# Optimization experiments

Measured on AMD Instinct MI355X. Metric: run time of the kernel, lower is better.

## Reference

```python
import jax, jax.numpy as jnp
import numpy as np

N = 50000        # nodes
E = 800_000      # edges (avg degree 16)
D_IN, D_HID, D_OUT = 512, 512, 256
P_DROP = 0.5


def setup_inputs() -> dict:
    key = jax.random.key(0)
    k0, k1, k2, k3 = jax.random.split(key, 4)
    x = jax.random.normal(k0, (N, D_IN), dtype=jnp.float32)
    edge_index = jax.random.randint(k1, (2, E), 0, N, dtype=jnp.int64)
    W1 = jax.random.normal(k2, (D_HID, D_IN), dtype=jnp.float32) * 0.02
    b1 = jnp.zeros((D_HID,), dtype=jnp.float32)
    W2 = jax.random.normal(k3, (D_OUT, D_HID), dtype=jnp.float32) * 0.02
    b2 = jnp.zeros((D_OUT,), dtype=jnp.float32)
    return {"x": x, "edge_index": edge_index, "W1": W1, "b1": b1, "W2": W2, "b2": b2}


def _gcn_norm(edge_index, n):
    # add self loops, then symmetric GCN normalization: D^-1/2 (A+I) D^-1/2
    src, dst = edge_index[0], edge_index[1]
    loops = jnp.arange(n, dtype=src.dtype)
    src = jnp.concatenate([src, loops])
    dst = jnp.concatenate([dst, loops])
    deg = jax.ops.segment_sum(jnp.ones_like(src, dtype=jnp.float32), dst, num_segments=n)
    dinv = jax.lax.rsqrt(deg)  # deg >= 1 because of self loops
    norm = dinv[src] * dinv[dst]  # [E+N]
    return src, dst, norm


def _propagate(x, src, dst, norm):
    # out[i] = sum_{(j->i)} norm_e * x[j]
    return jax.ops.segment_sum(x[src] * norm[:, None], dst, num_segments=x.shape[0])


def reference(x, edge_index, W1, b1, W2, b2):
    src, dst, norm = _gcn_norm(edge_index, x.shape[0])
    # SGConv layer 1 (K=1): propagate then linear
    h = _propagate(x, src, dst, norm) @ W1.T + b1
    h = jax.nn.relu(h)
    # F.dropout(p) with training=True default -> deterministic fixed-key mask here
    keep = jax.random.bernoulli(jax.random.key(42), 1.0 - P_DROP, h.shape)
    embedding = jnp.where(keep, h / (1.0 - P_DROP), 0.0)
    # SGConv layer 2
    out = _propagate(embedding, src, dst, norm) @ W2.T + b2
    return embedding, out
```

## Files before the change

### kernel.cpp

```cpp
#include <hip/hip_runtime.h>

typedef unsigned short u16t;
typedef __attribute__((ext_vector_type(8))) short short8;
typedef __attribute__((ext_vector_type(4))) float f32x4;
typedef __attribute__((ext_vector_type(4))) unsigned short u16x4;

__device__ __forceinline__ float bf2f(short b) {
  return __uint_as_float(((unsigned)(unsigned short)b) << 16);
}
__device__ __forceinline__ u16t f2bf(float f) {
  unsigned u = __float_as_uint(f);
  u += 0x7FFFu + ((u >> 16) & 1u);
  return (u16t)(u >> 16);
}

__device__ __forceinline__ bool keep_mask(unsigned flat) {
  const unsigned k0 = 0u, k1 = 42u;
  const unsigned k2 = k0 ^ k1 ^ 0x1BD11BDAu;
  unsigned x0 = 0u + k0;
  unsigned x1 = flat + k1;
#define TF_R(r) { x0 += x1; x1 = (x1 << r) | (x1 >> (32 - r)); x1 ^= x0; }
  TF_R(13) TF_R(15) TF_R(26) TF_R(6)  x0 += k1; x1 += k2 + 1u;
  TF_R(17) TF_R(29) TF_R(16) TF_R(24) x0 += k2; x1 += k0 + 2u;
  TF_R(13) TF_R(15) TF_R(26) TF_R(6)  x0 += k0; x1 += k1 + 3u;
  TF_R(17) TF_R(29) TF_R(16) TF_R(24) x0 += k1; x1 += k2 + 4u;
  TF_R(13) TF_R(15) TF_R(26) TF_R(6)  x0 += k2; x1 += k0 + 5u;
#undef TF_R
  return ((x0 ^ x1) >> 31) == 0u;
}

__device__ __forceinline__ void load_lds16(const u16t* g, u16t* l) {
  __builtin_amdgcn_global_load_lds((__attribute__((address_space(1))) void*)g,
                                   (__attribute__((address_space(3))) void*)l,
                                   16, 0, 0);
}

__global__ void cvt_bf16(const float* __restrict__ s, u16t* __restrict__ d, int n) {
  int i = (blockIdx.x * 256 + threadIdx.x) * 4;
  if (i < n) {
    f32x4 v = *(const f32x4*)&s[i];
    u16x4 o = { f2bf(v.x), f2bf(v.y), f2bf(v.z), f2bf(v.w) };
    *(u16x4*)&d[i] = o;
  }
}

__global__ void count_edges(const int* __restrict__ dst, int E, int* __restrict__ cnt) {
  int e = blockIdx.x * 256 + threadIdx.x;
  if (e < E) atomicAdd(&cnt[dst[e]], 1);
}

__global__ __launch_bounds__(256) void rowp_build(const int* __restrict__ cnt,
    int* __restrict__ rowp, int* __restrict__ cursor, float* __restrict__ dinv,
    int* __restrict__ gctr, int n) {
  __shared__ int sd[256];
  __shared__ int sbase;
  const int tid = threadIdx.x;
  const int i = blockIdx.x * 256 + tid;
  int c = (i < n) ? cnt[i] : 0;
  int v = c;
  sd[tid] = v;
  __syncthreads();
  for (int o = 1; o < 256; o <<= 1) {
    int t = (tid >= o) ? sd[tid - o] : 0;
    __syncthreads();
    v += t;
    sd[tid] = v;
    __syncthreads();
  }
  if (tid == 255) sbase = atomicAdd(gctr, v);
  __syncthreads();
  if (i < n) {
    int start = sbase + v - c;
    rowp[i] = start;
    cursor[i] = start;
    dinv[i] = rsqrtf((float)(c + 1));
  }
}

__global__ void fill_csr(const int* __restrict__ src, const int* __restrict__ dst, int E,
                         int* __restrict__ cursor, int* __restrict__ col) {
  int e = blockIdx.x * 256 + threadIdx.x;
  if (e < E) {
    int d = dst[e];
    int pos = atomicAdd(&cursor[d], 1);
    col[pos] = src[e];
  }
}

__global__ __launch_bounds__(256) void gemm_bt(const u16t* __restrict__ A,
                                               const u16t* __restrict__ B,
                                               u16t* __restrict__ C,
                                               int K, int Ncols) {
  __shared__ __align__(16) u16t lA[128 * 32];
  __shared__ __align__(16) u16t lB[128 * 32];
  const int tid = threadIdx.x;
  const int wave = tid >> 6, lane = tid & 63;
  const int wm = (wave & 1) * 64, wn = (wave >> 1) * 64;
  const int lrow = lane & 15, lq = lane >> 4;
  const u16t* Ab = A + (size_t)blockIdx.y * 128 * K;
  const u16t* Bb = B + (size_t)blockIdx.x * 128 * K;
  const int r0 = tid >> 2, c0 = (tid & 3) * 8;
  const int ldsOff = __builtin_amdgcn_readfirstlane((tid >> 6) * 512);

  f32x4 acc[4][4];
  const f32x4 zero = {0.f, 0.f, 0.f, 0.f};
#pragma unroll
  for (int mi = 0; mi < 4; ++mi)
#pragma unroll
    for (int ni = 0; ni < 4; ++ni) acc[mi][ni] = zero;

  for (int kt = 0; kt < K; kt += 32) {
    __syncthreads();
    load_lds16(Ab + (size_t)r0 * K + kt + c0, &lA[ldsOff]);
    load_lds16(Ab + (size_t)(r0 + 64) * K + kt + c0, &lA[2048 + ldsOff]);
    load_lds16(Bb + (size_t)r0 * K + kt + c0, &lB[ldsOff]);
    load_lds16(Bb + (size_t)(r0 + 64) * K + kt + c0, &lB[2048 + ldsOff]);
    __syncthreads();
    short8 af[4], bfr[4];
#pragma unroll
    for (int mi = 0; mi < 4; ++mi)
      af[mi] = *(const short8*)&lA[(wm + mi * 16 + lrow) * 32 + lq * 8];
#pragma unroll
    for (int ni = 0; ni < 4; ++ni)
      bfr[ni] = *(const short8*)&lB[(wn + ni * 16 + lrow) * 32 + lq * 8];
#pragma unroll
    for (int mi = 0; mi < 4; ++mi)
#pragma unroll
      for (int ni = 0; ni < 4; ++ni)
        acc[mi][ni] = __builtin_amdgcn_mfma_f32_16x16x32_bf16(af[mi], bfr[ni], acc[mi][ni], 0, 0, 0);
  }

  const size_t crow = (size_t)blockIdx.y * 128 + wm + lq * 4;
  const int ccol = blockIdx.x * 128 + wn + lrow;
#pragma unroll
  for (int mi = 0; mi < 4; ++mi)
#pragma unroll
    for (int r = 0; r < 4; ++r)
#pragma unroll
      for (int ni = 0; ni < 4; ++ni)
        C[(crow + mi * 16 + r) * Ncols + ccol + ni * 16] = f2bf(acc[mi][ni][r]);
}

__global__ __launch_bounds__(256) void prop1_kernel(const u16t* __restrict__ y1,
    const int* __restrict__ col, const int* __restrict__ rowp, const int* __restrict__ rowend,
    const float* __restrict__ dinv, const float* __restrict__ b1,
    float* __restrict__ embf, u16t* __restrict__ embb, int n) {
  const int lane = threadIdx.x & 63;
  const int i = blockIdx.x * 4 + (threadIdx.x >> 6);
  if (i >= n) return;
  const int f = lane * 8;
  const float di = dinv[i];
  float acc[8];
  short8 v = *(const short8*)&y1[(size_t)i * 512 + f];
#pragma unroll
  for (int j = 0; j < 8; ++j) acc[j] = di * bf2f(v[j]);
  int e = rowp[i];
  const int e1 = rowend[i];
  for (; e + 8 <= e1; e += 8) {
    int s[8];
    float w[8];
    short8 u[8];
#pragma unroll
    for (int q = 0; q < 8; ++q) s[q] = col[e + q];
#pragma unroll
    for (int q = 0; q < 8; ++q) w[q] = dinv[s[q]];
#pragma unroll
    for (int q = 0; q < 8; ++q) u[q] = *(const short8*)&y1[(size_t)s[q] * 512 + f];
#pragma unroll
    for (int q = 0; q < 8; ++q)
#pragma unroll
      for (int j = 0; j < 8; ++j) acc[j] += w[q] * bf2f(u[q][j]);
  }
  for (; e + 4 <= e1; e += 4) {
    int s[4];
    float w[4];
    short8 u[4];
#pragma unroll
    for (int q = 0; q < 4; ++q) s[q] = col[e + q];
#pragma unroll
    for (int q = 0; q < 4; ++q) w[q] = dinv[s[q]];
#pragma unroll
    for (int q = 0; q < 4; ++q) u[q] = *(const short8*)&y1[(size_t)s[q] * 512 + f];
#pragma unroll
    for (int q = 0; q < 4; ++q)
#pragma unroll
      for (int j = 0; j < 8; ++j) acc[j] += w[q] * bf2f(u[q][j]);
  }
  for (; e < e1; ++e) {
    const int s = col[e];
    const float w = dinv[s];
    short8 u = *(const short8*)&y1[(size_t)s * 512 + f];
#pragma unroll
    for (int j = 0; j < 8; ++j) acc[j] += w * bf2f(u[j]);
  }
  const unsigned flat = (unsigned)i * 512u + (unsigned)f;
  f32x4 o0, o1;
  short8 ob;
#pragma unroll
  for (int j = 0; j < 8; ++j) {
    float h = di * acc[j] + b1[f + j];
    h = fmaxf(h, 0.f);
    float eb = keep_mask(flat + (unsigned)j) ? 2.f * h : 0.f;
    if (j < 4) o0[j] = eb; else o1[j - 4] = eb;
    ob[j] = (short)f2bf(eb);
  }
  *(f32x4*)&embf[(size_t)i * 512 + f] = o0;
  *(f32x4*)&embf[(size_t)i * 512 + f + 4] = o1;
  *(short8*)&embb[(size_t)i * 512 + f] = ob;
}

__global__ __launch_bounds__(256) void prop2_kernel(const u16t* __restrict__ z,
    const int* __restrict__ col, const int* __restrict__ rowp, const int* __restrict__ rowend,
    const float* __restrict__ dinv, const float* __restrict__ b2,
    float* __restrict__ outp, int n) {
  const int h = threadIdx.x & 31;
  const int i = blockIdx.x * 8 + (threadIdx.x >> 5);
  if (i >= n) return;
  const int f = h * 8;
  const float di = dinv[i];
  float acc[8];
  short8 v = *(const short8*)&z[(size_t)i * 256 + f];
#pragma unroll
  for (int j = 0; j < 8; ++j) acc[j] = di * bf2f(v[j]);
  int e = rowp[i];
  const int e1 = rowend[i];
  for (; e + 4 <= e1; e += 4) {
    int s[4];
    float w[4];
    short8 u[4];
#pragma unroll
    for (int q = 0; q < 4; ++q) s[q] = col[e + q];
#pragma unroll
    for (int q = 0; q < 4; ++q) w[q] = dinv[s[q]];
#pragma unroll
    for (int q = 0; q < 4; ++q) u[q] = *(const short8*)&z[(size_t)s[q] * 256 + f];
#pragma unroll
    for (int q = 0; q < 4; ++q)
#pragma unroll
      for (int j = 0; j < 8; ++j) acc[j] += w[q] * bf2f(u[q][j]);
  }
  for (; e < e1; ++e) {
    const int s = col[e];
    const float w = dinv[s];
    short8 u = *(const short8*)&z[(size_t)s * 256 + f];
#pragma unroll
    for (int j = 0; j < 8; ++j) acc[j] += w * bf2f(u[j]);
  }
  f32x4 o0, o1;
#pragma unroll
  for (int j = 0; j < 8; ++j) {
    float r = di * acc[j] + b2[f + j];
    if (j < 4) o0[j] = r; else o1[j - 4] = r;
  }
  *(f32x4*)&outp[(size_t)i * 256 + f] = o0;
  *(f32x4*)&outp[(size_t)i * 256 + f + 4] = o1;
}

extern "C" void kernel_launch(void* const* d_in, const int* in_sizes, int n_in,
                              void* d_out, int out_size, void* d_ws, size_t ws_size,
                              hipStream_t stream) {
  (void)n_in; (void)out_size; (void)ws_size;
  const float* x  = (const float*)d_in[0];
  const int*   ei = (const int*)d_in[1];
  const float* W1 = (const float*)d_in[2];
  const float* b1 = (const float*)d_in[3];
  const float* W2 = (const float*)d_in[4];
  const float* b2 = (const float*)d_in[5];

  const int Nn = in_sizes[0] / 512;
  const int E  = in_sizes[1] / 2;
  const int Mpad = ((Nn + 127) / 128) * 128;
  const int K = 512;

  char* ws = (char*)d_ws;
  size_t off = 0;
  auto take = [&](size_t bytes) -> char* {
    char* p = ws + off;
    off += (bytes + 255) & ~(size_t)255;
    return p;
  };
  u16t* xb   = (u16t*)take((size_t)Mpad * 512 * 2);
  u16t* y1b  = (u16t*)take((size_t)Mpad * 512 * 2);
  u16t* W1b  = (u16t*)take((size_t)512 * 512 * 2);
  u16t* W2b  = (u16t*)take((size_t)256 * 512 * 2);
  int*   cnt    = (int*)take((size_t)(Nn + 1) * 4);
  int*   rowp   = (int*)take((size_t)Nn * 4);
  int*   cursor = (int*)take((size_t)Nn * 4);
  float* dinv   = (float*)take((size_t)Nn * 4);
  int*   colA   = (int*)take((size_t)E * 4);

  float* embf = (float*)d_out;
  float* outf = (float*)d_out + (size_t)Nn * 512;

  hipMemsetAsync(cnt, 0, (size_t)(Nn + 1) * 4, stream);

  const int n1 = Nn * 512;
  cvt_bf16<<<(n1 / 4 + 255) / 256, 256, 0, stream>>>(x, xb, n1);
  cvt_bf16<<<(512 * 512 / 4 + 255) / 256, 256, 0, stream>>>(W1, W1b, 512 * 512);
  cvt_bf16<<<(256 * 512 / 4 + 255) / 256, 256, 0, stream>>>(W2, W2b, 256 * 512);

  count_edges<<<(E + 255) / 256, 256, 0, stream>>>(ei + E, E, cnt);
  rowp_build<<<(Nn + 255) / 256, 256, 0, stream>>>(cnt, rowp, cursor, dinv, cnt + Nn, Nn);
  fill_csr<<<(E + 255) / 256, 256, 0, stream>>>(ei, ei + E, E, cursor, colA);

  dim3 g1(512 / 128, Mpad / 128);
  gemm_bt<<<g1, 256, 0, stream>>>(xb, W1b, y1b, K, 512);
  prop1_kernel<<<(Nn + 3) / 4, 256, 0, stream>>>(y1b, colA, rowp, cursor, dinv, b1,
                                                 embf, xb , Nn);

  u16t* zb = y1b;
  dim3 g2(256 / 128, Mpad / 128);
  gemm_bt<<<g2, 256, 0, stream>>>(xb, W2b, zb, K, 256);
  prop2_kernel<<<(Nn + 7) / 8, 256, 0, stream>>>(zb, colA, rowp, cursor, dinv, b2, outf, Nn);
}
```

Measured before the change: 591.4 us.

## Split propagation feature dimension across two blocks per node chunk

Both propagation kernels now split each node's feature row into two halves handled by separate blocks. The block index is remapped so that the two halves of a 4-node chunk are launched close together and can share L2 hits on the gathered neighbor rows. Each thread now loads narrower vectors (4 or 2 bf16 values), which doubles the block count and the parallelism available for hiding gather latency. The cost is that the edge indices and dinv values are read twice, and the narrower loads are less efficient per request. prop2 also moves from 32-thread to 64-thread groups per node and gains an 8-way unrolled edge loop.

New measurement: 590.9 us. About the same (-0.1%).

```diff
diff --git a/kernel.cpp b/kernel.cpp
--- a/kernel.cpp
+++ b/kernel.cpp
@@ -2,7 +2,10 @@
 
 typedef unsigned short u16t;
 typedef __attribute__((ext_vector_type(8))) short short8;
+typedef __attribute__((ext_vector_type(4))) short short4v;
+typedef __attribute__((ext_vector_type(2))) short short2v;
 typedef __attribute__((ext_vector_type(4))) float f32x4;
+typedef __attribute__((ext_vector_type(2))) float f32x2;
 typedef __attribute__((ext_vector_type(4))) unsigned short u16x4;
 
 __device__ __forceinline__ float bf2f(short b) {
@@ -144,116 +147,116 @@
 __global__ __launch_bounds__(256) void prop1_kernel(const u16t* __restrict__ y1,
     const int* __restrict__ col, const int* __restrict__ rowp, const int* __restrict__ rowend,
     const float* __restrict__ dinv, const float* __restrict__ b1,
-    float* __restrict__ embf, u16t* __restrict__ embb, int n) {
+    float* __restrict__ embf, u16t* __restrict__ embb, int n, int nchunk) {
+  const int b = blockIdx.x;
+  const int slot = b & 7;
+  const int hf = slot >> 2;
+  const int chunk = (b >> 3) * 4 + (slot & 3);
+  if (chunk >= nchunk) return;
+  const int i = __builtin_amdgcn_readfirstlane(chunk * 4 + (threadIdx.x >> 6));
+  if (i >= n) return;
   const int lane = threadIdx.x & 63;
-  const int i = blockIdx.x * 4 + (threadIdx.x >> 6);
-  if (i >= n) return;
-  const int f = lane * 8;
+  const int f = hf * 256 + lane * 4;
+
   const float di = dinv[i];
-  float acc[8];
-  short8 v = *(const short8*)&y1[(size_t)i * 512 + f];
-#pragma unroll
-  for (int j = 0; j < 8; ++j) acc[j] = di * bf2f(v[j]);
-  int e = rowp[i];
+  const int e0 = rowp[i];
   const int e1 = rowend[i];
+
+  float acc[4];
+  short4v v = *(const short4v*)&y1[(size_t)i * 512 + f];
+#pragma unroll
+  for (int j = 0; j < 4; ++j) acc[j] = di * bf2f(v[j]);
+
+  int e = e0;
   for (; e + 8 <= e1; e += 8) {
     int s[8];
     float w[8];
-    short8 u[8];
+    short4v u[8];
 #pragma unroll
     for (int q = 0; q < 8; ++q) s[q] = col[e + q];
 #pragma unroll
     for (int q = 0; q < 8; ++q) w[q] = dinv[s[q]];
 #pragma unroll
-    for (int q = 0; q < 8; ++q) u[q] = *(const short8*)&y1[(size_t)s[q] * 512 + f];
+    for (int q = 0; q < 8; ++q) u[q] = *(const short4v*)&y1[(size_t)s[q] * 512 + f];
 #pragma unroll
     for (int q = 0; q < 8; ++q)
 #pragma unroll
-      for (int j = 0; j < 8; ++j) acc[j] += w[q] * bf2f(u[q][j]);
-  }
-  for (; e + 4 <= e1; e += 4) {
-    int s[4];
-    float w[4];
-    short8 u[4];
-#pragma unroll
-    for (int q = 0; q < 4; ++q) s[q] = col[e + q];
-#pragma unroll
-    for (int q = 0; q < 4; ++q) w[q] = dinv[s[q]];
-#pragma unroll
-    for (int q = 0; q < 4; ++q) u[q] = *(const short8*)&y1[(size_t)s[q] * 512 + f];
-#pragma unroll
-    for (int q = 0; q < 4; ++q)
-#pragma unroll
-      for (int j = 0; j < 8; ++j) acc[j] += w[q] * bf2f(u[q][j]);
+      for (int j = 0; j < 4; ++j) acc[j] += w[q] * bf2f(u[q][j]);
   }
   for (; e < e1; ++e) {
     const int s = col[e];
     const float w = dinv[s];
-    short8 u = *(const short8*)&y1[(size_t)s * 512 + f];
-#pragma unroll
-    for (int j = 0; j < 8; ++j) acc[j] += w * bf2f(u[j]);
-  }
+    short4v u = *(const short4v*)&y1[(size_t)s * 512 + f];
+#pragma unroll
+    for (int j = 0; j < 4; ++j) acc[j] += w * bf2f(u[j]);
+  }
+
   const unsigned flat = (unsigned)i * 512u + (unsigned)f;
-  f32x4 o0, o1;
-  short8 ob;
-#pragma unroll
-  for (int j = 0; j < 8; ++j) {
+  f32x4 o;
+  short4v ob;
+#pragma unroll
+  for (int j = 0; j < 4; ++j) {
     float h = di * acc[j] + b1[f + j];
     h = fmaxf(h, 0.f);
     float eb = keep_mask(flat + (unsigned)j) ? 2.f * h : 0.f;
-    if (j < 4) o0[j] = eb; else o1[j - 4] = eb;
+    o[j] = eb;
     ob[j] = (short)f2bf(eb);
   }
-  *(f32x4*)&embf[(size_t)i * 512 + f] = o0;
-  *(f32x4*)&embf[(size_t)i * 512 + f + 4] = o1;
-  *(short8*)&embb[(size_t)i * 512 + f] = ob;
+  *(f32x4*)&embf[(size_t)i * 512 + f] = o;
+  *(short4v*)&embb[(size_t)i * 512 + f] = ob;
 }
 
 __global__ __launch_bounds__(256) void prop2_kernel(const u16t* __restrict__ z,
     const int* __restrict__ col, const int* __restrict__ rowp, const int* __restrict__ rowend,
     const float* __restrict__ dinv, const float* __restrict__ b2,
-    float* __restrict__ outp, int n) {
-  const int h = threadIdx.x & 31;
-  const int i = blockIdx.x * 8 + (threadIdx.x >> 5);
+    float* __restrict__ outp, int n, int nchunk) {
+  const int b = blockIdx.x;
+  const int slot = b & 7;
+  const int hf = slot >> 2;
+  const int chunk = (b >> 3) * 4 + (slot & 3);
+  if (chunk >= nchunk) return;
+  const int i = __builtin_amdgcn_readfirstlane(chunk * 4 + (threadIdx.x >> 6));
   if (i >= n) return;
-  const int f = h * 8;
+  const int lane = threadIdx.x & 63;
+  const int f = hf * 128 + lane * 2;
+
   const float di = dinv[i];
-  float acc[8];
-  short8 v = *(const short8*)&z[(size_t)i * 256 + f];
-#pragma unroll
-  for (int j = 0; j < 8; ++j) acc[j] = di * bf2f(v[j]);
-  int e = rowp[i];
+  const int e0 = rowp[i];
   const int e1 = rowend[i];
-  for (; e + 4 <= e1; e += 4) {
-    int s[4];
-    float w[4];
-    short8 u[4];
-#pragma unroll
-    for (int q = 0; q < 4; ++q) s[q] = col[e + q];
-#pragma unroll
-    for (int q = 0; q < 4; ++q) w[q] = dinv[s[q]];
-#pragma unroll
-    for (int q = 0; q < 4; ++q) u[q] = *(const short8*)&z[(size_t)s[q] * 256 + f];
-#pragma unroll
-    for (int q = 0; q < 4; ++q)
-#pragma unroll
-      for (int j = 0; j < 8; ++j) acc[j] += w[q] * bf2f(u[q][j]);
+
+  float acc[2];
+  short2v v = *(const short2v*)&z[(size_t)i * 256 + f];
+#pragma unroll
+  for (int j = 0; j < 2; ++j) acc[j] = di * bf2f(v[j]);
+
+  int e = e0;
+  for (; e + 8 <= e1; e += 8) {
+    int s[8];
+    float w[8];
+    short2v u[8];
+#pragma unroll
+    for (int q = 0; q < 8; ++q) s[q] = col[e + q];
+#pragma unroll
+    for (int q = 0; q < 8; ++q) w[q] = dinv[s[q]];
+#pragma unroll
+    for (int q = 0; q < 8; ++q) u[q] = *(const short2v*)&z[(size_t)s[q] * 256 + f];
+#pragma unroll
+    for (int q = 0; q < 8; ++q)
+#pragma unroll
+      for (int j = 0; j < 2; ++j) acc[j] += w[q] * bf2f(u[q][j]);
   }
   for (; e < e1; ++e) {
     const int s = col[e];
     const float w = dinv[s];
-    short8 u = *(const short8*)&z[(size_t)s * 256 + f];
-#pragma unroll
-    for (int j = 0; j < 8; ++j) acc[j] += w * bf2f(u[j]);
-  }
-  f32x4 o0, o1;
-#pragma unroll
-  for (int j = 0; j < 8; ++j) {
-    float r = di * acc[j] + b2[f + j];
-    if (j < 4) o0[j] = r; else o1[j - 4] = r;
-  }
-  *(f32x4*)&outp[(size_t)i * 256 + f] = o0;
-  *(f32x4*)&outp[(size_t)i * 256 + f + 4] = o1;
+    short2v u = *(const short2v*)&z[(size_t)s * 256 + f];
+#pragma unroll
+    for (int j = 0; j < 2; ++j) acc[j] += w * bf2f(u[j]);
+  }
+
+  f32x2 o;
+#pragma unroll
+  for (int j = 0; j < 2; ++j) o[j] = di * acc[j] + b2[f + j];
+  *(f32x2*)&outp[(size_t)i * 256 + f] = o;
 }
 
 extern "C" void kernel_launch(void* const* d_in, const int* in_sizes, int n_in,
@@ -303,13 +306,16 @@
   rowp_build<<<(Nn + 255) / 256, 256, 0, stream>>>(cnt, rowp, cursor, dinv, cnt + Nn, Nn);
   fill_csr<<<(E + 255) / 256, 256, 0, stream>>>(ei, ei + E, E, cursor, colA);
 
+  const int nchunk = (Nn + 3) / 4;
+  const int nblk_split = ((nchunk + 3) / 4) * 8;
+
   dim3 g1(512 / 128, Mpad / 128);
   gemm_bt<<<g1, 256, 0, stream>>>(xb, W1b, y1b, K, 512);
-  prop1_kernel<<<(Nn + 3) / 4, 256, 0, stream>>>(y1b, colA, rowp, cursor, dinv, b1,
-                                                 embf, xb , Nn);
+  prop1_kernel<<<nblk_split, 256, 0, stream>>>(y1b, colA, rowp, cursor, dinv, b1,
+                                               embf, xb , Nn, nchunk);
 
   u16t* zb = y1b;
   dim3 g2(256 / 128, Mpad / 128);
   gemm_bt<<<g2, 256, 0, stream>>>(xb, W2b, zb, K, 256);
-  prop2_kernel<<<(Nn + 7) / 8, 256, 0, stream>>>(zb, colA, rowp, cursor, dinv, b2, outf, Nn);
-}
+  prop2_kernel<<<nblk_split, 256, 0, stream>>>(zb, colA, rowp, cursor, dinv, b2, outf, Nn, nchunk);
+}
```
